# Kernel tuning notes

Hardware: AMD Instinct MI355X
Metric: run time of the kernel (lower is better)

## Reference

```python
import jax, jax.numpy as jnp
import numpy as np
import math

B, SQ, SK, D = 16, 2048, 2048, 64


def setup_inputs() -> dict:
    key = jax.random.key(0)
    kq, kk, kv, kl = jax.random.split(key, 4)
    queries = jax.random.normal(kq, (B, SQ, D), dtype=jnp.float32)
    keys = jax.random.normal(kk, (B, SK, D), dtype=jnp.float32)
    values = jax.random.normal(kv, (B, SK, D), dtype=jnp.float32)
    # valid key lengths in [1, SK]
    valid_lens = jax.random.randint(kl, (B,), 1, SK + 1, dtype=jnp.int32)
    return {"queries": queries, "keys": keys, "values": values, "valid_lens": valid_lens}


def reference(queries, keys, values, valid_lens):
    d = queries.shape[-1]
    # [B, SQ, SK] raw scores
    scores = jnp.einsum("bqd,bkd->bqk", queries, keys) / math.sqrt(d)
    # masked_softmax: key positions >= valid_len are set to -1e6 (d2l semantics)
    kpos = jnp.arange(scores.shape[-1], dtype=jnp.int32)  # [SK]
    mask = kpos[None, None, :] < valid_lens[:, None, None]  # [B,1,SK] -> broadcast
    scores = jnp.where(mask, scores, jnp.float32(-1e6))
    attn = jax.nn.softmax(scores, axis=-1)
    # dropout rate is 0.0 -> identity
    return jnp.einsum("bqk,bkd->bqd", attn, values)
```

## Files before the change

kernel.cpp:

```cpp
#include <hip/hip_runtime.h>

#define NB 16
#define SQL 2048
#define SKL 2048
#define DH 64
#define NSPLIT 8
#define CHUNK 256

typedef __attribute__((ext_vector_type(8)))  short bf16x8;
typedef __attribute__((ext_vector_type(4)))  unsigned short u16x4;
typedef __attribute__((ext_vector_type(8)))  unsigned short u16x8;
typedef __attribute__((ext_vector_type(4)))  float f32x4;
typedef __attribute__((ext_vector_type(16))) float f32x16;

#define LOG2E 1.4426950408889634f
#define K1 (0.125f * LOG2E)

__device__ __forceinline__ unsigned short f2bf(float f) {
    unsigned int u = __builtin_bit_cast(unsigned int, f);
    u += 0x7fffu + ((u >> 16) & 1u);
    return (unsigned short)(u >> 16);
}
__device__ __forceinline__ float bf2f(unsigned short h) {
    return __builtin_bit_cast(float, (unsigned int)h << 16);
}

__global__ __launch_bounds__(256) void prep_kernel(
    const float* __restrict__ Q, const float* __restrict__ K,
    const float* __restrict__ V,
    unsigned short* __restrict__ Qb, unsigned short* __restrict__ Kb,
    unsigned short* __restrict__ Vt) {
    const int blk = blockIdx.x;
    if (blk < 2048) {
        const float* src = (blk < 1024) ? Q : K;
        unsigned short* dst = (blk < 1024) ? Qb : Kb;
        const size_t base = ((size_t)(blk & 1023) * 256 + threadIdx.x) * 8;
        float4 a = *(const float4*)(src + base);
        float4 b = *(const float4*)(src + base + 4);
        u16x8 o;
        o[0] = f2bf(a.x); o[1] = f2bf(a.y); o[2] = f2bf(a.z); o[3] = f2bf(a.w);
        o[4] = f2bf(b.x); o[5] = f2bf(b.y); o[6] = f2bf(b.z); o[7] = f2bf(b.w);
        *(u16x8*)(dst + base) = o;
    } else {
        const int t  = blk - 2048;
        const int b  = t >> 5;
        const int kb = (t & 31) << 6;
        __shared__ float tile[64][65];
        const int tid = threadIdx.x;
        {
            const int r  = tid >> 2;
            const int cg = (tid & 3) << 4;
            const float* vsrc = V + ((size_t)b * SKL + (kb + r)) * DH;
            #pragma unroll
            for (int i = 0; i < 4; ++i) {
                float4 x = *(const float4*)(vsrc + cg + i * 4);
                tile[r][cg + i*4 + 0] = x.x;
                tile[r][cg + i*4 + 1] = x.y;
                tile[r][cg + i*4 + 2] = x.z;
                tile[r][cg + i*4 + 3] = x.w;
            }
        }
        __syncthreads();
        {
            const int d  = tid >> 2;
            const int kg = (tid & 3) << 4;
            unsigned short* dst = Vt + ((size_t)b * DH + d) * SKL + kb + kg;
            u16x8 o0, o1;
            #pragma unroll
            for (int j = 0; j < 8; ++j) o0[j] = f2bf(tile[kg + j][d]);
            #pragma unroll
            for (int j = 0; j < 8; ++j) o1[j] = f2bf(tile[kg + 8 + j][d]);
            *(u16x8*)(dst)     = o0;
            *(u16x8*)(dst + 8) = o1;
        }
    }
}

__global__ __launch_bounds__(256, 3) void attn_kernel(
    const unsigned short* __restrict__ Qb,
    const unsigned short* __restrict__ Kb,
    const unsigned short* __restrict__ Vt,
    const int* __restrict__ valid_lens,
    unsigned short* __restrict__ Opart,
    float2* __restrict__ MLpart) {
    const int qblk  = blockIdx.x;
    const int split = blockIdx.y;
    const int b     = blockIdx.z;

    const int valid  = valid_lens[b];
    const int kstart = split * CHUNK;
    if (kstart >= valid) return;
    const int kend   = (valid < kstart + CHUNK) ? valid : (kstart + CHUNK);
    const int ntiles = (kend - kstart + 63) >> 6;

    const int tid  = threadIdx.x;
    const int wave = tid >> 6;
    const int lane = tid & 63;
    const int l31  = lane & 31;
    const int h2   = lane >> 5;
    const int sw   = l31 & 7;

    __shared__ unsigned short Klds[64][64];
    __shared__ unsigned short Vlds[64][64];
    __shared__ unsigned short Plds[4][32][64];

    const int q0 = qblk * 128 + wave * 32;
    const unsigned short* qptr = Qb + ((size_t)b * SQL + q0 + l31) * DH + h2 * 8;
    bf16x8 qf[4];
    #pragma unroll
    for (int ks = 0; ks < 4; ++ks) qf[ks] = *(const bf16x8*)(qptr + ks * 16);

    const unsigned short* kbase = Kb + (size_t)b * SKL * DH;
    const unsigned short* vbase = Vt + (size_t)b * DH * SKL;

    f32x16 o[2];
    #pragma unroll
    for (int i = 0; i < 2; ++i)
        #pragma unroll
        for (int r = 0; r < 16; ++r) o[i][r] = 0.f;
    float mrow = -1e30f, lrow = 0.f;

    u16x8 kreg[2], vreg[2];
    #pragma unroll
    for (int i = 0; i < 2; ++i) {
        const int c = i * 256 + tid, r = c >> 3, col = (c & 7) << 3;
        kreg[i] = *(const u16x8*)(kbase + (size_t)(kstart + r) * DH + col);
        vreg[i] = *(const u16x8*)(vbase + (size_t)r * SKL + kstart + col);
    }

    for (int kt = 0; kt < ntiles; ++kt) {
        const int kb = kstart + (kt << 6);
        __syncthreads();
        #pragma unroll
        for (int i = 0; i < 2; ++i) {
            const int c = i * 256 + tid, r = c >> 3;
            const int pc = ((c & 7) ^ (r & 7)) << 3;
            *(u16x8*)&Klds[r][pc] = kreg[i];
            *(u16x8*)&Vlds[r][pc] = vreg[i];
        }
        __syncthreads();
        if (kt + 1 < ntiles) {
            const int kn = kb + 64;
            #pragma unroll
            for (int i = 0; i < 2; ++i) {
                const int c = i * 256 + tid, r = c >> 3, col = (c & 7) << 3;
                kreg[i] = *(const u16x8*)(kbase + (size_t)(kn + r) * DH + col);
                vreg[i] = *(const u16x8*)(vbase + (size_t)r * SKL + kn + col);
            }
        }

        f32x16 s[2];
        #pragma unroll
        for (int t = 0; t < 2; ++t) {
            #pragma unroll
            for (int r = 0; r < 16; ++r) s[t][r] = 0.f;
            #pragma unroll
            for (int ks = 0; ks < 4; ++ks) {
                const bf16x8 kf = *(const bf16x8*)
                    &Klds[t * 32 + l31][((2 * ks + h2) ^ sw) << 3];
                s[t] = __builtin_amdgcn_mfma_f32_32x32x16_bf16(kf, qf[ks], s[t], 0, 0, 0);
            }
        }

        if (kb + 64 > kend) {
            #pragma unroll
            for (int t = 0; t < 2; ++t)
                #pragma unroll
                for (int r = 0; r < 16; ++r)
                    if (kb + t * 32 + (r & 3) + 8 * (r >> 2) + 4 * h2 >= kend)
                        s[t][r] = -1e30f;
        }

        float tmax = -1e30f;
        #pragma unroll
        for (int t = 0; t < 2; ++t)
            #pragma unroll
            for (int r = 0; r < 16; ++r) tmax = fmaxf(tmax, s[t][r]);
        tmax = fmaxf(tmax, __shfl_xor(tmax, 32));

        const float mnew  = fmaxf(mrow, 0.125f * tmax);
        const float alpha = exp2f((mrow - mnew) * LOG2E);
        const float mk    = mnew * LOG2E;
        float rs = 0.f;
        #pragma unroll
        for (int t = 0; t < 2; ++t)
            #pragma unroll
            for (int r = 0; r < 16; ++r) {
                const float p = exp2f(fmaf(s[t][r], K1, -mk));
                s[t][r] = p;
                rs += p;
            }
        rs += __shfl_xor(rs, 32);
        lrow = lrow * alpha + rs;
        mrow = mnew;
        #pragma unroll
        for (int i = 0; i < 2; ++i)
            #pragma unroll
            for (int r = 0; r < 16; ++r) o[i][r] *= alpha;

        #pragma unroll
        for (int t = 0; t < 2; ++t)
            #pragma unroll
            for (int g = 0; g < 4; ++g) {
                u16x4 pw;
                pw[0] = f2bf(s[t][g * 4 + 0]); pw[1] = f2bf(s[t][g * 4 + 1]);
                pw[2] = f2bf(s[t][g * 4 + 2]); pw[3] = f2bf(s[t][g * 4 + 3]);
                const int unit = (4 * t + g) ^ sw;
                *(u16x4*)&Plds[wave][l31][(unit << 3) + (h2 << 2)] = pw;
            }
        bf16x8 pf[4];
        #pragma unroll
        for (int ks = 0; ks < 4; ++ks)
            pf[ks] = *(const bf16x8*)&Plds[wave][l31][((2 * ks + h2) ^ sw) << 3];

        #pragma unroll
        for (int dt = 0; dt < 2; ++dt)
            #pragma unroll
            for (int ks = 0; ks < 4; ++ks) {
                const bf16x8 vf = *(const bf16x8*)
                    &Vlds[dt * 32 + l31][((2 * ks + h2) ^ sw) << 3];
                o[dt] = __builtin_amdgcn_mfma_f32_32x32x16_bf16(vf, pf[ks], o[dt], 0, 0, 0);
            }
    }

    unsigned short* op = Opart +
        (((size_t)b * NSPLIT + split) * SQL + q0 + l31) * DH;
    #pragma unroll
    for (int dt = 0; dt < 2; ++dt)
        #pragma unroll
        for (int g = 0; g < 4; ++g) {
            u16x4 ow;
            ow[0] = f2bf(o[dt][g * 4 + 0]); ow[1] = f2bf(o[dt][g * 4 + 1]);
            ow[2] = f2bf(o[dt][g * 4 + 2]); ow[3] = f2bf(o[dt][g * 4 + 3]);
            *(u16x4*)(op + dt * 32 + 8 * g + 4 * h2) = ow;
        }
    if (h2 == 0)
        MLpart[((size_t)b * NSPLIT + split) * SQL + q0 + l31] =
            make_float2(mrow, lrow);
}

__global__ __launch_bounds__(256) void reduce_kernel(
    const unsigned short* __restrict__ Opart, const float2* __restrict__ MLpart,
    const int* __restrict__ valid_lens, float* __restrict__ out) {
    const int b   = blockIdx.y;
    const int tid = threadIdx.x;
    const int q   = blockIdx.x * 64 + (tid >> 2);
    const int dg  = (tid & 3) << 4;
    const int ns  = (valid_lens[b] + CHUNK - 1) / CHUNK;

    float m[NSPLIT], l[NSPLIT];
    float M = -1e30f;
    for (int s = 0; s < ns; ++s) {
        float2 ml = MLpart[((size_t)b * NSPLIT + s) * SQL + q];
        m[s] = ml.x; l[s] = ml.y;
        M = fmaxf(M, ml.x);
    }
    float L = 0.f;
    float acc[16];
    #pragma unroll
    for (int i = 0; i < 16; ++i) acc[i] = 0.f;
    for (int s = 0; s < ns; ++s) {
        const float w = exp2f((m[s] - M) * LOG2E);
        L += l[s] * w;
        const unsigned short* p =
            Opart + (((size_t)b * NSPLIT + s) * SQL + q) * DH + dg;
        u16x8 a0 = *(const u16x8*)(p);
        u16x8 a1 = *(const u16x8*)(p + 8);
        #pragma unroll
        for (int i = 0; i < 8; ++i) acc[i]     += w * bf2f(a0[i]);
        #pragma unroll
        for (int i = 0; i < 8; ++i) acc[8 + i] += w * bf2f(a1[i]);
    }
    const float inv = 1.0f / L;
    float* op = out + ((size_t)b * SQL + q) * DH + dg;
    f32x4 ov;
    #pragma unroll
    for (int i = 0; i < 4; ++i) {
        ov[0] = acc[i*4+0] * inv; ov[1] = acc[i*4+1] * inv;
        ov[2] = acc[i*4+2] * inv; ov[3] = acc[i*4+3] * inv;
        *(f32x4*)(op + i * 4) = ov;
    }
}

extern "C" void kernel_launch(void* const* d_in, const int* in_sizes, int n_in,
                              void* d_out, int out_size, void* d_ws, size_t ws_size,
                              hipStream_t stream) {
    const float* Q  = (const float*)d_in[0];
    const float* K  = (const float*)d_in[1];
    const float* V  = (const float*)d_in[2];
    const int*   vl = (const int*)d_in[3];
    float* out = (float*)d_out;

    unsigned short* Qb = (unsigned short*)d_ws;
    unsigned short* Kb = Qb + (size_t)NB * SQL * DH;
    unsigned short* Vt = Kb + (size_t)NB * SKL * DH;
    unsigned short* Opart = Vt + (size_t)NB * SKL * DH;
    float2* MLpart = (float2*)(Opart + (size_t)NB * NSPLIT * SQL * DH);

    prep_kernel<<<dim3(2560), dim3(256), 0, stream>>>(Q, K, V, Qb, Kb, Vt);
    attn_kernel<<<dim3(SQL / 128, NSPLIT, NB), dim3(256), 0, stream>>>(
        Qb, Kb, Vt, vl, Opart, MLpart);
    reduce_kernel<<<dim3(SQL / 64, NB), dim3(256), 0, stream>>>(
        Opart, MLpart, vl, out);
}
```

Measured before the change: 110.8 us.

## Fuse split-K reduction into attention kernel via last-block atomic counter

Drops the separate reduce kernel launch. Each attention block increments a per-(batch, query-block) counter, and the last split to finish merges all partial outputs into the final result. When a batch needs only one split, the block normalizes and writes fp32 output directly, skipping the partial buffer. In exchange it adds a memset launch, threadfences and atomics, and the reduction now runs on one block per query tile, which may load-balance less evenly.

Result: slower. 307.5 us (+177.6%).

```diff
diff --git a/kernel.cpp b/kernel.cpp
--- a/kernel.cpp
+++ b/kernel.cpp
@@ -6,6 +6,7 @@
 #define DH 64
 #define NSPLIT 8
 #define CHUNK 256
+#define NQBLK (SQL / 128)
 
 typedef __attribute__((ext_vector_type(8)))  short bf16x8;
 typedef __attribute__((ext_vector_type(4)))  unsigned short u16x4;
@@ -82,7 +83,9 @@
     const unsigned short* __restrict__ Vt,
     const int* __restrict__ valid_lens,
     unsigned short* __restrict__ Opart,
-    float2* __restrict__ MLpart) {
+    float2* __restrict__ MLpart,
+    unsigned int* __restrict__ cnt,
+    float* __restrict__ out) {
     const int qblk  = blockIdx.x;
     const int split = blockIdx.y;
     const int b     = blockIdx.z;
@@ -90,8 +93,9 @@
     const int valid  = valid_lens[b];
     const int kstart = split * CHUNK;
     if (kstart >= valid) return;
-    const int kend   = (valid < kstart + CHUNK) ? valid : (kstart + CHUNK);
-    const int ntiles = (kend - kstart + 63) >> 6;
+    const int kend    = (valid < kstart + CHUNK) ? valid : (kstart + CHUNK);
+    const int ntiles  = (kend - kstart + 63) >> 6;
+    const int nactive = (valid + CHUNK - 1) / CHUNK;
 
     const int tid  = threadIdx.x;
     const int wave = tid >> 6;
@@ -103,6 +107,7 @@
     __shared__ unsigned short Klds[64][64];
     __shared__ unsigned short Vlds[64][64];
     __shared__ unsigned short Plds[4][32][64];
+    __shared__ int red_flag;
 
     const int q0 = qblk * 128 + wave * 32;
     const unsigned short* qptr = Qb + ((size_t)b * SQL + q0 + l31) * DH + h2 * 8;
@@ -223,6 +228,21 @@
             }
     }
 
+    if (nactive == 1) {
+        const float inv = 1.0f / lrow;
+        float* op = out + ((size_t)b * SQL + q0 + l31) * DH;
+        #pragma unroll
+        for (int dt = 0; dt < 2; ++dt)
+            #pragma unroll
+            for (int g = 0; g < 4; ++g) {
+                f32x4 ov;
+                ov[0] = o[dt][g*4+0] * inv; ov[1] = o[dt][g*4+1] * inv;
+                ov[2] = o[dt][g*4+2] * inv; ov[3] = o[dt][g*4+3] * inv;
+                *(f32x4*)(op + dt * 32 + 8 * g + 4 * h2) = ov;
+            }
+        return;
+    }
+
     unsigned short* op = Opart +
         (((size_t)b * NSPLIT + split) * SQL + q0 + l31) * DH;
     #pragma unroll
@@ -237,48 +257,50 @@
     if (h2 == 0)
         MLpart[((size_t)b * NSPLIT + split) * SQL + q0 + l31] =
             make_float2(mrow, lrow);
-}
-
-__global__ __launch_bounds__(256) void reduce_kernel(
-    const unsigned short* __restrict__ Opart, const float2* __restrict__ MLpart,
-    const int* __restrict__ valid_lens, float* __restrict__ out) {
-    const int b   = blockIdx.y;
-    const int tid = threadIdx.x;
-    const int q   = blockIdx.x * 64 + (tid >> 2);
-    const int dg  = (tid & 3) << 4;
-    const int ns  = (valid_lens[b] + CHUNK - 1) / CHUNK;
+
+    __threadfence();
+    if (tid == 0) {
+        unsigned int old = atomicAdd(&cnt[b * NQBLK + qblk], 1u);
+        red_flag = (old == (unsigned int)(nactive - 1));
+    }
+    __syncthreads();
+    if (!red_flag) return;
+    __threadfence();
+
+    const int q  = qblk * 128 + (tid >> 1);
+    const int dh = (tid & 1) << 5;
 
     float m[NSPLIT], l[NSPLIT];
     float M = -1e30f;
-    for (int s = 0; s < ns; ++s) {
-        float2 ml = MLpart[((size_t)b * NSPLIT + s) * SQL + q];
-        m[s] = ml.x; l[s] = ml.y;
+    for (int s2 = 0; s2 < nactive; ++s2) {
+        float2 ml = MLpart[((size_t)b * NSPLIT + s2) * SQL + q];
+        m[s2] = ml.x; l[s2] = ml.y;
         M = fmaxf(M, ml.x);
     }
     float L = 0.f;
-    float acc[16];
-    #pragma unroll
-    for (int i = 0; i < 16; ++i) acc[i] = 0.f;
-    for (int s = 0; s < ns; ++s) {
-        const float w = exp2f((m[s] - M) * LOG2E);
-        L += l[s] * w;
+    float acc[32];
+    #pragma unroll
+    for (int i = 0; i < 32; ++i) acc[i] = 0.f;
+    for (int s2 = 0; s2 < nactive; ++s2) {
+        const float w = exp2f((m[s2] - M) * LOG2E);
+        L += l[s2] * w;
         const unsigned short* p =
-            Opart + (((size_t)b * NSPLIT + s) * SQL + q) * DH + dg;
-        u16x8 a0 = *(const u16x8*)(p);
-        u16x8 a1 = *(const u16x8*)(p + 8);
-        #pragma unroll
-        for (int i = 0; i < 8; ++i) acc[i]     += w * bf2f(a0[i]);
-        #pragma unroll
-        for (int i = 0; i < 8; ++i) acc[8 + i] += w * bf2f(a1[i]);
+            Opart + (((size_t)b * NSPLIT + s2) * SQL + q) * DH + dh;
+        #pragma unroll
+        for (int i = 0; i < 4; ++i) {
+            u16x8 a = *(const u16x8*)(p + i * 8);
+            #pragma unroll
+            for (int j = 0; j < 8; ++j) acc[i * 8 + j] += w * bf2f(a[j]);
+        }
     }
     const float inv = 1.0f / L;
-    float* op = out + ((size_t)b * SQL + q) * DH + dg;
-    f32x4 ov;
-    #pragma unroll
-    for (int i = 0; i < 4; ++i) {
+    float* outp = out + ((size_t)b * SQL + q) * DH + dh;
+    #pragma unroll
+    for (int i = 0; i < 8; ++i) {
+        f32x4 ov;
         ov[0] = acc[i*4+0] * inv; ov[1] = acc[i*4+1] * inv;
         ov[2] = acc[i*4+2] * inv; ov[3] = acc[i*4+3] * inv;
-        *(f32x4*)(op + i * 4) = ov;
+        *(f32x4*)(outp + i * 4) = ov;
     }
 }
 
@@ -296,10 +318,10 @@
     unsigned short* Vt = Kb + (size_t)NB * SKL * DH;
     unsigned short* Opart = Vt + (size_t)NB * SKL * DH;
     float2* MLpart = (float2*)(Opart + (size_t)NB * NSPLIT * SQL * DH);
-
+    unsigned int* cnt = (unsigned int*)(MLpart + (size_t)NB * NSPLIT * SQL);
+
+    (void)hipMemsetAsync(cnt, 0, NB * NQBLK * sizeof(unsigned int), stream);
     prep_kernel<<<dim3(2560), dim3(256), 0, stream>>>(Q, K, V, Qb, Kb, Vt);
-    attn_kernel<<<dim3(SQL / 128, NSPLIT, NB), dim3(256), 0, stream>>>(
-        Qb, Kb, Vt, vl, Opart, MLpart);
-    reduce_kernel<<<dim3(SQL / 64, NB), dim3(256), 0, stream>>>(
-        Opart, MLpart, vl, out);
-}
+    attn_kernel<<<dim3(NQBLK, NSPLIT, NB), dim3(256), 0, stream>>>(
+        Qb, Kb, Vt, vl, Opart, MLpart, cnt, out);
+}
```

## Fuse Q/K bf16 conversion into attention and write output directly for single-split batches

Applied to the files above, without the earlier changes.

The prep kernel now only transposes V. The attention kernel loads fp32 Q and K and converts them to bf16 in registers before storing to LDS, which removes a separate pass over Q and K and its workspace traffic. For batches whose valid length fits in one split, the attention kernel normalizes and writes the final fp32 output directly, and the reduce kernel skips those batches. In exchange, K global loads double in size and each K tile is converted once per q-block rather than once overall.

Result: no change. 111.1 us (+0.3%).

```diff
diff --git a/kernel.cpp b/kernel.cpp
--- a/kernel.cpp
+++ b/kernel.cpp
@@ -24,65 +24,56 @@
 __device__ __forceinline__ float bf2f(unsigned short h) {
     return __builtin_bit_cast(float, (unsigned int)h << 16);
 }
+__device__ __forceinline__ bf16x8 pack8(float4 a, float4 b) {
+    u16x8 o;
+    o[0] = f2bf(a.x); o[1] = f2bf(a.y); o[2] = f2bf(a.z); o[3] = f2bf(a.w);
+    o[4] = f2bf(b.x); o[5] = f2bf(b.y); o[6] = f2bf(b.z); o[7] = f2bf(b.w);
+    return __builtin_bit_cast(bf16x8, o);
+}
 
 __global__ __launch_bounds__(256) void prep_kernel(
-    const float* __restrict__ Q, const float* __restrict__ K,
-    const float* __restrict__ V,
-    unsigned short* __restrict__ Qb, unsigned short* __restrict__ Kb,
-    unsigned short* __restrict__ Vt) {
-    const int blk = blockIdx.x;
-    if (blk < 2048) {
-        const float* src = (blk < 1024) ? Q : K;
-        unsigned short* dst = (blk < 1024) ? Qb : Kb;
-        const size_t base = ((size_t)(blk & 1023) * 256 + threadIdx.x) * 8;
-        float4 a = *(const float4*)(src + base);
-        float4 b = *(const float4*)(src + base + 4);
-        u16x8 o;
-        o[0] = f2bf(a.x); o[1] = f2bf(a.y); o[2] = f2bf(a.z); o[3] = f2bf(a.w);
-        o[4] = f2bf(b.x); o[5] = f2bf(b.y); o[6] = f2bf(b.z); o[7] = f2bf(b.w);
-        *(u16x8*)(dst + base) = o;
-    } else {
-        const int t  = blk - 2048;
-        const int b  = t >> 5;
-        const int kb = (t & 31) << 6;
-        __shared__ float tile[64][65];
-        const int tid = threadIdx.x;
-        {
-            const int r  = tid >> 2;
-            const int cg = (tid & 3) << 4;
-            const float* vsrc = V + ((size_t)b * SKL + (kb + r)) * DH;
-            #pragma unroll
-            for (int i = 0; i < 4; ++i) {
-                float4 x = *(const float4*)(vsrc + cg + i * 4);
-                tile[r][cg + i*4 + 0] = x.x;
-                tile[r][cg + i*4 + 1] = x.y;
-                tile[r][cg + i*4 + 2] = x.z;
-                tile[r][cg + i*4 + 3] = x.w;
-            }
-        }
-        __syncthreads();
-        {
-            const int d  = tid >> 2;
-            const int kg = (tid & 3) << 4;
-            unsigned short* dst = Vt + ((size_t)b * DH + d) * SKL + kb + kg;
-            u16x8 o0, o1;
-            #pragma unroll
-            for (int j = 0; j < 8; ++j) o0[j] = f2bf(tile[kg + j][d]);
-            #pragma unroll
-            for (int j = 0; j < 8; ++j) o1[j] = f2bf(tile[kg + 8 + j][d]);
-            *(u16x8*)(dst)     = o0;
-            *(u16x8*)(dst + 8) = o1;
-        }
+    const float* __restrict__ V, unsigned short* __restrict__ Vt) {
+    const int t  = blockIdx.x;
+    const int b  = t >> 5;
+    const int kb = (t & 31) << 6;
+    __shared__ float tile[64][65];
+    const int tid = threadIdx.x;
+    {
+        const int r  = tid >> 2;
+        const int cg = (tid & 3) << 4;
+        const float* vsrc = V + ((size_t)b * SKL + (kb + r)) * DH;
+        #pragma unroll
+        for (int i = 0; i < 4; ++i) {
+            float4 x = *(const float4*)(vsrc + cg + i * 4);
+            tile[r][cg + i*4 + 0] = x.x;
+            tile[r][cg + i*4 + 1] = x.y;
+            tile[r][cg + i*4 + 2] = x.z;
+            tile[r][cg + i*4 + 3] = x.w;
+        }
+    }
+    __syncthreads();
+    {
+        const int d  = tid >> 2;
+        const int kg = (tid & 3) << 4;
+        unsigned short* dst = Vt + ((size_t)b * DH + d) * SKL + kb + kg;
+        u16x8 o0, o1;
+        #pragma unroll
+        for (int j = 0; j < 8; ++j) o0[j] = f2bf(tile[kg + j][d]);
+        #pragma unroll
+        for (int j = 0; j < 8; ++j) o1[j] = f2bf(tile[kg + 8 + j][d]);
+        *(u16x8*)(dst)     = o0;
+        *(u16x8*)(dst + 8) = o1;
     }
 }
 
 __global__ __launch_bounds__(256, 3) void attn_kernel(
-    const unsigned short* __restrict__ Qb,
-    const unsigned short* __restrict__ Kb,
+    const float* __restrict__ Q,
+    const float* __restrict__ K,
     const unsigned short* __restrict__ Vt,
     const int* __restrict__ valid_lens,
     unsigned short* __restrict__ Opart,
-    float2* __restrict__ MLpart) {
+    float2* __restrict__ MLpart,
+    float* __restrict__ out) {
     const int qblk  = blockIdx.x;
     const int split = blockIdx.y;
     const int b     = blockIdx.z;
@@ -90,8 +81,9 @@
     const int valid  = valid_lens[b];
     const int kstart = split * CHUNK;
     if (kstart >= valid) return;
-    const int kend   = (valid < kstart + CHUNK) ? valid : (kstart + CHUNK);
-    const int ntiles = (kend - kstart + 63) >> 6;
+    const int kend    = (valid < kstart + CHUNK) ? valid : (kstart + CHUNK);
+    const int ntiles  = (kend - kstart + 63) >> 6;
+    const int nactive = (valid + CHUNK - 1) / CHUNK;
 
     const int tid  = threadIdx.x;
     const int wave = tid >> 6;
@@ -105,12 +97,14 @@
     __shared__ unsigned short Plds[4][32][64];
 
     const int q0 = qblk * 128 + wave * 32;
-    const unsigned short* qptr = Qb + ((size_t)b * SQL + q0 + l31) * DH + h2 * 8;
+    const float* qptr = Q + ((size_t)b * SQL + q0 + l31) * DH + h2 * 8;
     bf16x8 qf[4];
     #pragma unroll
-    for (int ks = 0; ks < 4; ++ks) qf[ks] = *(const bf16x8*)(qptr + ks * 16);
-
-    const unsigned short* kbase = Kb + (size_t)b * SKL * DH;
+    for (int ks = 0; ks < 4; ++ks)
+        qf[ks] = pack8(*(const float4*)(qptr + ks * 16),
+                       *(const float4*)(qptr + ks * 16 + 4));
+
+    const float* kbase = K + (size_t)b * SKL * DH;
     const unsigned short* vbase = Vt + (size_t)b * DH * SKL;
 
     f32x16 o[2];
@@ -120,11 +114,13 @@
         for (int r = 0; r < 16; ++r) o[i][r] = 0.f;
     float mrow = -1e30f, lrow = 0.f;
 
-    u16x8 kreg[2], vreg[2];
+    float4 kra[2], krb[2];
+    u16x8  vreg[2];
     #pragma unroll
     for (int i = 0; i < 2; ++i) {
         const int c = i * 256 + tid, r = c >> 3, col = (c & 7) << 3;
-        kreg[i] = *(const u16x8*)(kbase + (size_t)(kstart + r) * DH + col);
+        kra[i]  = *(const float4*)(kbase + (size_t)(kstart + r) * DH + col);
+        krb[i]  = *(const float4*)(kbase + (size_t)(kstart + r) * DH + col + 4);
         vreg[i] = *(const u16x8*)(vbase + (size_t)r * SKL + kstart + col);
     }
 
@@ -135,8 +131,8 @@
         for (int i = 0; i < 2; ++i) {
             const int c = i * 256 + tid, r = c >> 3;
             const int pc = ((c & 7) ^ (r & 7)) << 3;
-            *(u16x8*)&Klds[r][pc] = kreg[i];
-            *(u16x8*)&Vlds[r][pc] = vreg[i];
+            *(bf16x8*)&Klds[r][pc] = pack8(kra[i], krb[i]);
+            *(u16x8*)&Vlds[r][pc]  = vreg[i];
         }
         __syncthreads();
         if (kt + 1 < ntiles) {
@@ -144,7 +140,8 @@
             #pragma unroll
             for (int i = 0; i < 2; ++i) {
                 const int c = i * 256 + tid, r = c >> 3, col = (c & 7) << 3;
-                kreg[i] = *(const u16x8*)(kbase + (size_t)(kn + r) * DH + col);
+                kra[i]  = *(const float4*)(kbase + (size_t)(kn + r) * DH + col);
+                krb[i]  = *(const float4*)(kbase + (size_t)(kn + r) * DH + col + 4);
                 vreg[i] = *(const u16x8*)(vbase + (size_t)r * SKL + kn + col);
             }
         }
@@ -223,6 +220,21 @@
             }
     }
 
+    if (nactive == 1) {
+        const float inv = 1.0f / lrow;
+        float* op = out + ((size_t)b * SQL + q0 + l31) * DH;
+        #pragma unroll
+        for (int dt = 0; dt < 2; ++dt)
+            #pragma unroll
+            for (int g = 0; g < 4; ++g) {
+                f32x4 ov;
+                ov[0] = o[dt][g*4+0] * inv; ov[1] = o[dt][g*4+1] * inv;
+                ov[2] = o[dt][g*4+2] * inv; ov[3] = o[dt][g*4+3] * inv;
+                *(f32x4*)(op + dt * 32 + 8 * g + 4 * h2) = ov;
+            }
+        return;
+    }
+
     unsigned short* op = Opart +
         (((size_t)b * NSPLIT + split) * SQL + q0 + l31) * DH;
     #pragma unroll
@@ -243,10 +255,11 @@
     const unsigned short* __restrict__ Opart, const float2* __restrict__ MLpart,
     const int* __restrict__ valid_lens, float* __restrict__ out) {
     const int b   = blockIdx.y;
+    const int ns  = (valid_lens[b] + CHUNK - 1) / CHUNK;
+    if (ns == 1) return;
     const int tid = threadIdx.x;
     const int q   = blockIdx.x * 64 + (tid >> 2);
     const int dg  = (tid & 3) << 4;
-    const int ns  = (valid_lens[b] + CHUNK - 1) / CHUNK;
 
     float m[NSPLIT], l[NSPLIT];
     float M = -1e30f;
@@ -291,15 +304,13 @@
     const int*   vl = (const int*)d_in[3];
     float* out = (float*)d_out;
 
-    unsigned short* Qb = (unsigned short*)d_ws;
-    unsigned short* Kb = Qb + (size_t)NB * SQL * DH;
-    unsigned short* Vt = Kb + (size_t)NB * SKL * DH;
+    unsigned short* Vt = (unsigned short*)d_ws;
     unsigned short* Opart = Vt + (size_t)NB * SKL * DH;
     float2* MLpart = (float2*)(Opart + (size_t)NB * NSPLIT * SQL * DH);
 
-    prep_kernel<<<dim3(2560), dim3(256), 0, stream>>>(Q, K, V, Qb, Kb, Vt);
+    prep_kernel<<<dim3(512), dim3(256), 0, stream>>>(V, Vt);
     attn_kernel<<<dim3(SQL / 128, NSPLIT, NB), dim3(256), 0, stream>>>(
-        Qb, Kb, Vt, vl, Opart, MLpart);
+        Q, K, Vt, vl, Opart, MLpart, out);
     reduce_kernel<<<dim3(SQL / 64, NB), dim3(256), 0, stream>>>(
         Opart, MLpart, vl, out);
 }
```
